# Kernel tuning notes

Hardware: AMD Instinct MI355X
Metric: run time of the kernel (lower is better)

The kernel has to match this reference:

```python
import jax, jax.numpy as jnp
import numpy as np

N_NODES = 100000
N_EDGES = 1200000
D = 64
N_LAYERS = 3


def setup_inputs() -> dict:
    key = jax.random.key(0)
    k0, k1, k2, k3, k4 = jax.random.split(key, 5)
    x = jax.random.normal(k0, (N_NODES, D), dtype=jnp.float32)
    edge_index = jax.random.randint(k1, (2, N_EDGES), 0, N_NODES, dtype=jnp.int32)
    edge_weight = jax.random.uniform(k2, (N_EDGES,), dtype=jnp.float32)
    # stacked per-layer params: 3 layers of 64->64
    self_kernels = jax.random.normal(k3, (N_LAYERS, D, D), dtype=jnp.float32) * 0.1
    neighbor_kernels = jax.random.normal(k4, (N_LAYERS, D, D), dtype=jnp.float32) * 0.1
    biases = jnp.zeros((N_LAYERS, D), dtype=jnp.float32)
    return {"x": x, "edge_index": edge_index, "edge_weight": edge_weight,
            "self_kernels": self_kernels, "neighbor_kernels": neighbor_kernels,
            "biases": biases}


def _sage_layer(h, row, col, edge_weight, self_k, neigh_k, b):
    # gather source-node features per edge, weight them: [E, d]
    msg = h[col] * edge_weight[:, None]
    # sum-aggregate messages at target nodes: [N, d]
    agg = jax.ops.segment_sum(msg, row, num_segments=N_NODES)
    # concat=False -> self transform + neighbor transform added, then relu
    out = h @ self_k + agg @ neigh_k + b
    return jax.nn.relu(out)


def reference(x, edge_index, edge_weight, self_kernels, neighbor_kernels, biases):
    row, col = edge_index[0], edge_index[1]
    h = x
    for i in range(N_LAYERS):
        h = _sage_layer(h, row, col, edge_weight,
                        self_kernels[i], neighbor_kernels[i], biases[i])
    return h
```

## Files before the change

### kernel.cpp

```cpp
#include <hip/hip_runtime.h>

#define NN 100000
#define NE 1200000
#define DD 64
#define NTILES 3125
#define NBK 391
#define MLEN (NBK * 256)
#define EPB 4688

typedef unsigned int uint32;
typedef unsigned char uint8;
typedef unsigned short ushort16;
typedef __attribute__((ext_vector_type(8))) short short8;
typedef __attribute__((ext_vector_type(16))) float f32x16;

__device__ __forceinline__ ushort16 f2bf(float x) {
    uint32 u = __float_as_uint(x);
    u += 0x7FFFu + ((u >> 16) & 1u);
    return (ushort16)(u >> 16);
}
__device__ __forceinline__ float bflo(uint32 u) { return __uint_as_float(u << 16); }
__device__ __forceinline__ float bfhi(uint32 u) { return __uint_as_float(u & 0xFFFF0000u); }
__device__ __forceinline__ uint32 pack2(float a, float b) {
    return (uint32)f2bf(a) | ((uint32)f2bf(b) << 16);
}


__global__ __launch_bounds__(512)
void k_bcount(const int* __restrict__ row, int* __restrict__ M) {
    __shared__ int bins[NBK];
    for (int i = threadIdx.x; i < NBK; i += 512) bins[i] = 0;
    __syncthreads();
    int start = blockIdx.x * EPB;
    int end = min(start + EPB, NE);
    for (int e = start + (int)threadIdx.x; e < end; e += 512)
        atomicAdd(&bins[row[e] >> 8], 1);
    __syncthreads();
    for (int i = threadIdx.x; i < NBK; i += 512)
        M[i * 256 + blockIdx.x] = bins[i];
}

__global__ void k_scan1(const int* __restrict__ in, int* __restrict__ outx,
                        int* __restrict__ partials) {
    __shared__ int tmp[256];
    int t = threadIdx.x;
    int i = blockIdx.x * 256 + t;
    int v = (i < MLEN) ? in[i] : 0;
    tmp[t] = v;
    __syncthreads();
    #pragma unroll
    for (int off = 1; off < 256; off <<= 1) {
        int add = (t >= off) ? tmp[t - off] : 0;
        __syncthreads();
        tmp[t] += add;
        __syncthreads();
    }
    if (i < MLEN) outx[i] = tmp[t] - v;
    if (t == 255) partials[blockIdx.x] = tmp[255];
}

__global__ void k_scan2(int* __restrict__ partials) {
    __shared__ int tmp[512];
    int t = threadIdx.x;
    int v = (t < NBK) ? partials[t] : 0;
    tmp[t] = v;
    __syncthreads();
    #pragma unroll
    for (int off = 1; off < 512; off <<= 1) {
        int add = (t >= off) ? tmp[t - off] : 0;
        __syncthreads();
        tmp[t] += add;
        __syncthreads();
    }
    if (t < NBK) partials[t] = tmp[t] - v;
}

__global__ void k_scan3(int* __restrict__ outx, const int* __restrict__ partials) {
    int i = blockIdx.x * 256 + threadIdx.x;
    if (i < MLEN) outx[i] += partials[i >> 8];
}

__global__ __launch_bounds__(512)
void k_bscatter(const int* __restrict__ row, const int* __restrict__ col,
                const float* __restrict__ ew, const int* __restrict__ Mscan,
                uint32* __restrict__ colw, uint8* __restrict__ rowlo) {
    __shared__ int cur[NBK];
    for (int i = threadIdx.x; i < NBK; i += 512)
        cur[i] = Mscan[i * 256 + blockIdx.x];
    __syncthreads();
    int start = blockIdx.x * EPB;
    int end = min(start + EPB, NE);
    for (int e = start + (int)threadIdx.x; e < end; e += 512) {
        int r = row[e];
        int wq = (int)(ew[e] * 32767.0f + 0.5f);
        wq = (wq > 32767) ? 32767 : wq;
        int p = atomicAdd(&cur[r >> 8], 1);
        colw[p]  = ((uint32)col[e] << 15) | (uint32)wq;
        rowlo[p] = (uint8)(r & 255);
    }
}

__global__ __launch_bounds__(256)
void k_build(const int* __restrict__ Mscan, const uint32* __restrict__ colw,
             const uint8* __restrict__ rowlo,
             uint32* __restrict__ edges, int* __restrict__ offsets) {
    __shared__ int bins[256];
    __shared__ int tmp[256];
    __shared__ int cur[256];
    int b = blockIdx.x;
    int t = threadIdx.x;
    int bstart = Mscan[b * 256];
    int bend   = (b == NBK - 1) ? NE : Mscan[(b + 1) * 256];
    bins[t] = 0;
    __syncthreads();
    for (int p = bstart + t; p < bend; p += 256)
        atomicAdd(&bins[rowlo[p]], 1);
    __syncthreads();
    int v = bins[t];
    tmp[t] = v;
    __syncthreads();
    #pragma unroll
    for (int off = 1; off < 256; off <<= 1) {
        int add = (t >= off) ? tmp[t - off] : 0;
        __syncthreads();
        tmp[t] += add;
        __syncthreads();
    }
    int base = bstart + (tmp[t] - v);
    cur[t] = base;
    int rowid = b * 256 + t;
    if (rowid < NN) offsets[rowid] = base;
    if (b == 0 && t == 0) offsets[NN] = NE;
    __syncthreads();
    for (int p = bstart + t; p < bend; p += 256) {
        uint32 cw = colw[p];
        int dst = atomicAdd(&cur[rowlo[p]], 1);
        edges[dst] = cw;
    }
}


__global__ void k_packW(const float* __restrict__ selfk,
                        const float* __restrict__ neighk,
                        short8* __restrict__ wpack) {
    int tid = blockIdx.x * 256 + threadIdx.x;
    if (tid >= 3 * 16 * 64) return;
    int lane  = tid & 63;
    int frag  = (tid >> 6) & 15;
    int layer = tid >> 10;
    int g = frag >> 3;
    int t = (frag >> 2) & 1;
    int s = frag & 3;
    const float* W = (g ? neighk : selfk) + layer * 4096;
    int n = t * 32 + (lane & 31);
    int k0 = s * 16 + (lane >> 5) * 8;
    short8 v;
    #pragma unroll
    for (int j = 0; j < 8; j++) v[j] = (short)f2bf(W[(k0 + j) * 64 + n]);
    wpack[tid] = v;
}


template <bool IN_BF16>
__global__ __launch_bounds__(256)
void gemm_mfma(const void* __restrict__ h_, ushort16* __restrict__ hs,
               ushort16* __restrict__ y,
               const short8* __restrict__ wpack,
               const float* __restrict__ bias) {
    int lane  = threadIdx.x & 63;
    int wave  = threadIdx.x >> 6;
    int wid   = blockIdx.x * 4 + wave;
    int nwv   = gridDim.x * 4;
    int mrow  = lane & 31;
    int khalf = lane >> 5;
    int t     = wid & 1;

    short8 Wf[2][4];
    #pragma unroll
    for (int g = 0; g < 2; g++)
        #pragma unroll
        for (int s = 0; s < 4; s++)
            Wf[g][s] = wpack[(((g * 2 + t) * 4) + s) * 64 + lane];

    float bval = bias[t * 32 + mrow];

    for (int tile = wid >> 1; tile < NTILES; tile += nwv >> 1) {
        int n0 = tile * 32;

        short8 A[4];
        if (IN_BF16) {
            const short8* hb = (const short8*)h_;
            int base = (n0 + mrow) * 8 + khalf;
            #pragma unroll
            for (int s = 0; s < 4; s++) A[s] = hb[base + s * 2];
        } else {
            const float* hf = (const float*)h_ + (n0 + mrow) * 64 + khalf * 8;
            #pragma unroll
            for (int s = 0; s < 4; s++) {
                short8 a;
                #pragma unroll
                for (int j = 0; j < 8; j++) a[j] = (short)f2bf(hf[s * 16 + j]);
                A[s] = a;
            }
        }

        f32x16 acc0, acc1;
        #pragma unroll
        for (int r = 0; r < 16; r++) { acc0[r] = 0.f; acc1[r] = 0.f; }

        #pragma unroll
        for (int s = 0; s < 4; s++) {
            acc0 = __builtin_amdgcn_mfma_f32_32x32x16_bf16(A[s], Wf[0][s], acc0, 0, 0, 0);
            acc1 = __builtin_amdgcn_mfma_f32_32x32x16_bf16(A[s], Wf[1][s], acc1, 0, 0, 0);
        }

        int colbase = t * 32 + mrow;
        #pragma unroll
        for (int r = 0; r < 16; r++) {
            int rw = (r & 3) + 8 * (r >> 2) + 4 * khalf;
            int n = n0 + rw;
            hs[n * DD + colbase] = f2bf(acc0[r] + bval);
            y [n * DD + colbase] = f2bf(acc1[r]);
        }
    }
}


template <bool OUT_BF16>
__global__ __launch_bounds__(256)
void agg_kernel(const uint2* __restrict__ hs2, const uint2* __restrict__ y2,
                void* __restrict__ out, const int* __restrict__ offsets,
                const uint32* __restrict__ edges) {
    int lane = threadIdx.x & 63;
    int wave = threadIdx.x >> 6;
    int g  = lane >> 4;
    int fl = lane & 15;
    int n = (blockIdx.x * 4 + wave) * 4 + g;

    uint2 hv = hs2[n * 16 + fl];
    float a0 = bflo(hv.x), a1 = bfhi(hv.x), a2 = bflo(hv.y), a3 = bfhi(hv.y);

    int s = offsets[n], e = offsets[n + 1];
    #pragma unroll 4
    for (int j = s; j < e; j++) {
        uint32 ed = edges[j];
        int c = (int)(ed >> 15);
        float w = (float)(ed & 32767u) * (1.0f / 32767.0f);
        uint2 yv = y2[c * 16 + fl];
        a0 = fmaf(bflo(yv.x), w, a0);
        a1 = fmaf(bfhi(yv.x), w, a1);
        a2 = fmaf(bflo(yv.y), w, a2);
        a3 = fmaf(bfhi(yv.y), w, a3);
    }
    a0 = fmaxf(a0, 0.f); a1 = fmaxf(a1, 0.f);
    a2 = fmaxf(a2, 0.f); a3 = fmaxf(a3, 0.f);
    if (OUT_BF16) {
        uint2 o; o.x = pack2(a0, a1); o.y = pack2(a2, a3);
        ((uint2*)out)[n * 16 + fl] = o;
    } else {
        ((float4*)out)[n * 16 + fl] = make_float4(a0, a1, a2, a3);
    }
}


extern "C" void kernel_launch(void* const* d_in, const int* in_sizes, int n_in,
                              void* d_out, int out_size, void* d_ws, size_t ws_size,
                              hipStream_t stream) {
    const float* x      = (const float*)d_in[0];
    const int*   ei     = (const int*)d_in[1];
    const float* ew     = (const float*)d_in[2];
    const float* selfk  = (const float*)d_in[3];
    const float* neighk = (const float*)d_in[4];
    const float* biases = (const float*)d_in[5];
    float* out = (float*)d_out;

    char* w = (char*)d_ws;
    ushort16* hP    = (ushort16*)w; w += (size_t)NN * DD * sizeof(ushort16);
    ushort16* hsQ   = (ushort16*)w; w += (size_t)NN * DD * sizeof(ushort16);
    ushort16* yR    = (ushort16*)w; w += (size_t)NN * DD * sizeof(ushort16);
    uint32* edges   = (uint32*)w;   w += (size_t)NE * sizeof(uint32);
    uint32* colwB   = (uint32*)w;   w += (size_t)NE * sizeof(uint32);
    uint8*  rowlo   = (uint8*)w;    w += (size_t)NE * sizeof(uint8);
    w = (char*)(((size_t)w + 255) & ~(size_t)255);
    int*    M       = (int*)w;      w += (size_t)MLEN * sizeof(int);
    int*    Mscan   = (int*)w;      w += (size_t)MLEN * sizeof(int);
    int*    offsets = (int*)w;      w += (size_t)(NN + 1) * sizeof(int);
    int*    partials= (int*)w;      w += 512 * sizeof(int);
    short8* wpack   = (short8*)w;   w += (size_t)3 * 16 * 64 * sizeof(short8);

    const int* row = ei;
    const int* col = ei + NE;

    k_packW   <<<12, 256, 0, stream>>>(selfk, neighk, wpack);
    k_bcount  <<<256, 512, 0, stream>>>(row, M);
    k_scan1   <<<NBK, 256, 0, stream>>>(M, Mscan, partials);
    k_scan2   <<<1, 512, 0, stream>>>(partials);
    k_scan3   <<<NBK, 256, 0, stream>>>(Mscan, partials);
    k_bscatter<<<256, 512, 0, stream>>>(row, col, ew, Mscan, colwB, rowlo);
    k_build   <<<NBK, 256, 0, stream>>>(Mscan, colwB, rowlo, edges, offsets);

    int gemm_blocks = 782;
    int agg_blocks  = NN / 16;

    gemm_mfma<false><<<gemm_blocks, 256, 0, stream>>>(x, hsQ, yR, wpack, biases);
    agg_kernel<true><<<agg_blocks, 256, 0, stream>>>((const uint2*)hsQ, (const uint2*)yR, hP, offsets, edges);
    gemm_mfma<true> <<<gemm_blocks, 256, 0, stream>>>(hP, hsQ, yR, wpack + 1024, biases + 64);
    agg_kernel<true><<<agg_blocks, 256, 0, stream>>>((const uint2*)hsQ, (const uint2*)yR, hP, offsets, edges);
    gemm_mfma<true> <<<gemm_blocks, 256, 0, stream>>>(hP, hsQ, yR, wpack + 2048, biases + 128);
    agg_kernel<false><<<agg_blocks, 256, 0, stream>>>((const uint2*)hsQ, (const uint2*)yR, out, offsets, edges);
}
```

Measured before the change: 252.1 us.

## Fuse aggregation with next layer's GEMM and fold scan fixup into consumers

Layers 2 and 3 now run in one kernel per layer. It aggregates 32 nodes into shared memory as bf16, then applies the next layer's MFMA GEMM directly, so the bf16 h buffer no longer makes a round trip through global memory and two launches disappear. The scan-fixup kernel is also removed: the partial offsets are added inside bscatter and build instead. Ping-pong hs/y buffers replace the shared ones. In exchange, the fused kernel has a barrier between the irregular gather and the GEMM, and its per-block load balance depends on node degree.

```diff
diff --git a/kernel.cpp b/kernel.cpp
--- a/kernel.cpp
+++ b/kernel.cpp
@@ -75,18 +75,14 @@
     if (t < NBK) partials[t] = tmp[t] - v;
 }
 
-__global__ void k_scan3(int* __restrict__ outx, const int* __restrict__ partials) {
-    int i = blockIdx.x * 256 + threadIdx.x;
-    if (i < MLEN) outx[i] += partials[i >> 8];
-}
-
 __global__ __launch_bounds__(512)
 void k_bscatter(const int* __restrict__ row, const int* __restrict__ col,
                 const float* __restrict__ ew, const int* __restrict__ Mscan,
+                const int* __restrict__ partials,
                 uint32* __restrict__ colw, uint8* __restrict__ rowlo) {
     __shared__ int cur[NBK];
     for (int i = threadIdx.x; i < NBK; i += 512)
-        cur[i] = Mscan[i * 256 + blockIdx.x];
+        cur[i] = Mscan[i * 256 + blockIdx.x] + partials[i];
     __syncthreads();
     int start = blockIdx.x * EPB;
     int end = min(start + EPB, NE);
@@ -101,16 +97,16 @@
 }
 
 __global__ __launch_bounds__(256)
-void k_build(const int* __restrict__ Mscan, const uint32* __restrict__ colw,
-             const uint8* __restrict__ rowlo,
+void k_build(const int* __restrict__ Mscan, const int* __restrict__ partials,
+             const uint32* __restrict__ colw, const uint8* __restrict__ rowlo,
              uint32* __restrict__ edges, int* __restrict__ offsets) {
     __shared__ int bins[256];
     __shared__ int tmp[256];
     __shared__ int cur[256];
     int b = blockIdx.x;
     int t = threadIdx.x;
-    int bstart = Mscan[b * 256];
-    int bend   = (b == NBK - 1) ? NE : Mscan[(b + 1) * 256];
+    int bstart = Mscan[b * 256] + partials[b];
+    int bend   = (b == NBK - 1) ? NE : Mscan[(b + 1) * 256] + partials[b + 1];
     bins[t] = 0;
     __syncthreads();
     for (int p = bstart + t; p < bend; p += 256)
@@ -161,9 +157,8 @@
 }
 
 
-template <bool IN_BF16>
 __global__ __launch_bounds__(256)
-void gemm_mfma(const void* __restrict__ h_, ushort16* __restrict__ hs,
+void gemm_mfma(const float* __restrict__ hf_, ushort16* __restrict__ hs,
                ushort16* __restrict__ y,
                const short8* __restrict__ wpack,
                const float* __restrict__ bias) {
@@ -186,22 +181,14 @@
 
     for (int tile = wid >> 1; tile < NTILES; tile += nwv >> 1) {
         int n0 = tile * 32;
-
+        const float* hf = hf_ + (n0 + mrow) * 64 + khalf * 8;
         short8 A[4];
-        if (IN_BF16) {
-            const short8* hb = (const short8*)h_;
-            int base = (n0 + mrow) * 8 + khalf;
+        #pragma unroll
+        for (int s = 0; s < 4; s++) {
+            short8 a;
             #pragma unroll
-            for (int s = 0; s < 4; s++) A[s] = hb[base + s * 2];
-        } else {
-            const float* hf = (const float*)h_ + (n0 + mrow) * 64 + khalf * 8;
-            #pragma unroll
-            for (int s = 0; s < 4; s++) {
-                short8 a;
-                #pragma unroll
-                for (int j = 0; j < 8; j++) a[j] = (short)f2bf(hf[s * 16 + j]);
-                A[s] = a;
-            }
+            for (int j = 0; j < 8; j++) a[j] = (short)f2bf(hf[s * 16 + j]);
+            A[s] = a;
         }
 
         f32x16 acc0, acc1;
@@ -226,11 +213,79 @@
 }
 
 
-template <bool OUT_BF16>
 __global__ __launch_bounds__(256)
-void agg_kernel(const uint2* __restrict__ hs2, const uint2* __restrict__ y2,
-                void* __restrict__ out, const int* __restrict__ offsets,
-                const uint32* __restrict__ edges) {
+void agg_gemm(const uint2* __restrict__ hs2, const uint2* __restrict__ y2,
+              ushort16* __restrict__ hs_out, ushort16* __restrict__ y_out,
+              const int* __restrict__ offsets, const uint32* __restrict__ edges,
+              const short8* __restrict__ wpack, const float* __restrict__ bias) {
+    __shared__ uint32 sh[32 * 36];
+    int lane = threadIdx.x & 63;
+    int wave = threadIdx.x >> 6;
+    int g  = lane >> 4;
+    int fl = lane & 15;
+    int n0 = blockIdx.x * 32;
+
+    #pragma unroll
+    for (int q = 0; q < 2; q++) {
+        int lrow = wave * 8 + q * 4 + g;
+        int n = n0 + lrow;
+        uint2 hv = hs2[n * 16 + fl];
+        float a0 = bflo(hv.x), a1 = bfhi(hv.x), a2 = bflo(hv.y), a3 = bfhi(hv.y);
+        int s = offsets[n], e = offsets[n + 1];
+        #pragma unroll 4
+        for (int j = s; j < e; j++) {
+            uint32 ed = edges[j];
+            int c = (int)(ed >> 15);
+            float w = (float)(ed & 32767u) * (1.0f / 32767.0f);
+            uint2 yv = y2[c * 16 + fl];
+            a0 = fmaf(bflo(yv.x), w, a0);
+            a1 = fmaf(bfhi(yv.x), w, a1);
+            a2 = fmaf(bflo(yv.y), w, a2);
+            a3 = fmaf(bfhi(yv.y), w, a3);
+        }
+        sh[lrow * 36 + fl * 2]     = pack2(fmaxf(a0, 0.f), fmaxf(a1, 0.f));
+        sh[lrow * 36 + fl * 2 + 1] = pack2(fmaxf(a2, 0.f), fmaxf(a3, 0.f));
+    }
+    __syncthreads();
+
+    int mrow  = lane & 31;
+    int khalf = lane >> 5;
+    int gsel  = wave >> 1;
+    int t     = wave & 1;
+
+    short8 Wf[4];
+    #pragma unroll
+    for (int s = 0; s < 4; s++)
+        Wf[s] = wpack[(((gsel * 2 + t) * 4) + s) * 64 + lane];
+
+    short8 A[4];
+    #pragma unroll
+    for (int s = 0; s < 4; s++)
+        A[s] = *(const short8*)&sh[mrow * 36 + s * 8 + khalf * 4];
+
+    f32x16 acc;
+    #pragma unroll
+    for (int r = 0; r < 16; r++) acc[r] = 0.f;
+    #pragma unroll
+    for (int s = 0; s < 4; s++)
+        acc = __builtin_amdgcn_mfma_f32_32x32x16_bf16(A[s], Wf[s], acc, 0, 0, 0);
+
+    float bval = gsel ? 0.f : bias[t * 32 + mrow];
+    ushort16* dst = gsel ? y_out : hs_out;
+    int colbase = t * 32 + mrow;
+    #pragma unroll
+    for (int r = 0; r < 16; r++) {
+        int rw = (r & 3) + 8 * (r >> 2) + 4 * khalf;
+        int n = n0 + rw;
+        dst[n * DD + colbase] = f2bf(acc[r] + bval);
+    }
+}
+
+
+__global__ __launch_bounds__(256)
+void agg_final(const uint2* __restrict__ hs2, const uint2* __restrict__ y2,
+               float4* __restrict__ out, const int* __restrict__ offsets,
+               const uint32* __restrict__ edges) {
     int lane = threadIdx.x & 63;
     int wave = threadIdx.x >> 6;
     int g  = lane >> 4;
@@ -252,14 +307,8 @@
         a2 = fmaf(bflo(yv.y), w, a2);
         a3 = fmaf(bfhi(yv.y), w, a3);
     }
-    a0 = fmaxf(a0, 0.f); a1 = fmaxf(a1, 0.f);
-    a2 = fmaxf(a2, 0.f); a3 = fmaxf(a3, 0.f);
-    if (OUT_BF16) {
-        uint2 o; o.x = pack2(a0, a1); o.y = pack2(a2, a3);
-        ((uint2*)out)[n * 16 + fl] = o;
-    } else {
-        ((float4*)out)[n * 16 + fl] = make_float4(a0, a1, a2, a3);
-    }
+    out[n * 16 + fl] = make_float4(fmaxf(a0, 0.f), fmaxf(a1, 0.f),
+                                   fmaxf(a2, 0.f), fmaxf(a3, 0.f));
 }
 
 
@@ -275,9 +324,10 @@
     float* out = (float*)d_out;
 
     char* w = (char*)d_ws;
-    ushort16* hP    = (ushort16*)w; w += (size_t)NN * DD * sizeof(ushort16);
-    ushort16* hsQ   = (ushort16*)w; w += (size_t)NN * DD * sizeof(ushort16);
-    ushort16* yR    = (ushort16*)w; w += (size_t)NN * DD * sizeof(ushort16);
+    ushort16* hsA   = (ushort16*)w; w += (size_t)NN * DD * sizeof(ushort16);
+    ushort16* yA    = (ushort16*)w; w += (size_t)NN * DD * sizeof(ushort16);
+    ushort16* hsB   = (ushort16*)w; w += (size_t)NN * DD * sizeof(ushort16);
+    ushort16* yB    = (ushort16*)w; w += (size_t)NN * DD * sizeof(ushort16);
     uint32* edges   = (uint32*)w;   w += (size_t)NE * sizeof(uint32);
     uint32* colwB   = (uint32*)w;   w += (size_t)NE * sizeof(uint32);
     uint8*  rowlo   = (uint8*)w;    w += (size_t)NE * sizeof(uint8);
@@ -295,17 +345,16 @@
     k_bcount  <<<256, 512, 0, stream>>>(row, M);
     k_scan1   <<<NBK, 256, 0, stream>>>(M, Mscan, partials);
     k_scan2   <<<1, 512, 0, stream>>>(partials);
-    k_scan3   <<<NBK, 256, 0, stream>>>(Mscan, partials);
-    k_bscatter<<<256, 512, 0, stream>>>(row, col, ew, Mscan, colwB, rowlo);
-    k_build   <<<NBK, 256, 0, stream>>>(Mscan, colwB, rowlo, edges, offsets);
-
-    int gemm_blocks = 782;
-    int agg_blocks  = NN / 16;
-
-    gemm_mfma<false><<<gemm_blocks, 256, 0, stream>>>(x, hsQ, yR, wpack, biases);
-    agg_kernel<true><<<agg_blocks, 256, 0, stream>>>((const uint2*)hsQ, (const uint2*)yR, hP, offsets, edges);
-    gemm_mfma<true> <<<gemm_blocks, 256, 0, stream>>>(hP, hsQ, yR, wpack + 1024, biases + 64);
-    agg_kernel<true><<<agg_blocks, 256, 0, stream>>>((const uint2*)hsQ, (const uint2*)yR, hP, offsets, edges);
-    gemm_mfma<true> <<<gemm_blocks, 256, 0, stream>>>(hP, hsQ, yR, wpack + 2048, biases + 128);
-    agg_kernel<false><<<agg_blocks, 256, 0, stream>>>((const uint2*)hsQ, (const uint2*)yR, out, offsets, edges);
-}
+    k_bscatter<<<256, 512, 0, stream>>>(row, col, ew, Mscan, partials, colwB, rowlo);
+    k_build   <<<NBK, 256, 0, stream>>>(Mscan, partials, colwB, rowlo, edges, offsets);
+
+    gemm_mfma<<<782, 256, 0, stream>>>(x, hsA, yA, wpack, biases);
+    agg_gemm <<<NTILES, 256, 0, stream>>>((const uint2*)hsA, (const uint2*)yA,
+                                          hsB, yB, offsets, edges,
+                                          wpack + 1024, biases + 64);
+    agg_gemm <<<NTILES, 256, 0, stream>>>((const uint2*)hsB, (const uint2*)yB,
+                                          hsA, yA, offsets, edges,
+                                          wpack + 2048, biases + 128);
+    agg_final<<<NN / 16, 256, 0, stream>>>((const uint2*)hsA, (const uint2*)yA,
+                                           (float4*)out, offsets, edges);
+}
```

Result: faster. 232.5 us (-7.8%).
